# Optimization experiments

Measured on AMD Instinct MI355X. Metric: run time of the kernel, lower is better.

The kernel has to match this reference:

```python
import jax, jax.numpy as jnp
import numpy as np


def setup_inputs() -> dict:
    key = jax.random.key(0)
    k1, k2, k3, k4 = jax.random.split(key, 4)
    B, T, C, H = 16, 2048, 384, 64
    x = jax.random.normal(k1, (B, T, C), dtype=jnp.float32)
    Wq = jax.random.normal(k2, (C, H), dtype=jnp.float32) * (1.0 / np.sqrt(C))
    Wk = jax.random.normal(k3, (C, H), dtype=jnp.float32) * (1.0 / np.sqrt(C))
    Wv = jax.random.normal(k4, (C, H), dtype=jnp.float32) * (1.0 / np.sqrt(C))
    return {"x": x, "Wq": Wq, "Wk": Wk, "Wv": Wv}


def reference(x, Wq, Wk, Wv):
    # x: [B, T, C]; Wq/Wk/Wv: [C, H]
    T = x.shape[1]
    H = Wk.shape[1]
    q = jnp.einsum('btc,ch->bth', x, Wq)
    k = jnp.einsum('btc,ch->bth', x, Wk)
    v = jnp.einsum('btc,ch->bth', x, Wv)
    scale = 1.0 / jnp.sqrt(jnp.asarray(H, dtype=x.dtype))
    wei = jnp.einsum('bth,bsh->bts', q, k) * scale  # [B, T, T]
    causal = jnp.tril(jnp.ones((T, T), dtype=bool))
    wei = jnp.where(causal, wei, -jnp.inf)
    attn = jax.nn.softmax(wei, axis=-1)
    # dropout p=0 -> identity
    out = jnp.einsum('bts,bsh->bth', attn, v)  # [B, T, H]
    return out
```

## Files before the change

### kernel.cpp

```cpp
#include <hip/hip_runtime.h>
#include <hip/hip_bf16.h>

#define B_ 16
#define T_ 2048
#define C_ 384
#define H_ 64

typedef __attribute__((ext_vector_type(8))) short short8;
typedef __attribute__((ext_vector_type(4))) short short4_t;
typedef __attribute__((ext_vector_type(4))) float floatx4;
typedef __attribute__((ext_vector_type(2))) unsigned int uint2_t;
typedef __attribute__((ext_vector_type(4))) unsigned int uintx4;

#if defined(__has_builtin)
#if __has_builtin(__builtin_amdgcn_mfma_f32_16x16x16bf16_1k)
#define HAVE_MFMA16 1
#endif
#endif

static __device__ __forceinline__ short f2bf(float f) {
    unsigned u = __builtin_bit_cast(unsigned, f);
    u += 0x7FFF + ((u >> 16) & 1);
    return (short)(u >> 16);
}
static __device__ __forceinline__ float bf2f(short s) {
    return __builtin_bit_cast(float, ((unsigned)(unsigned short)s) << 16);
}
static __device__ __forceinline__ unsigned cvt_pk_bf16(float lo, float hi) {
    unsigned r;
    asm("v_cvt_pk_bf16_f32 %0, %1, %2" : "=v"(r) : "v"(lo), "v"(hi));
    return r;
}

__global__ void wt_kernel(const float* __restrict__ Wq, const float* __restrict__ Wk,
                          const float* __restrict__ Wv, short* __restrict__ wt2) {
    int idx = blockIdx.x * 256 + threadIdx.x;
    if (idx >= 12 * 12 * 512) return;
    int f = idx >> 9, within = idx & 511;
    int lane = within >> 3, jj = within & 7;
    int nt16 = f / 12, kc32 = f - nt16 * 12;
    int mat = nt16 >> 2, w = nt16 & 3;
    int quad = lane >> 4, l16 = lane & 15;
    int h = w * 16 + l16;
    int c = kc32 * 32 + quad * 8 + jj;
    const float* W = (mat == 0) ? Wq : ((mat == 1) ? Wk : Wv);
    wt2[idx] = f2bf(W[c * H_ + h]);
}

__global__ __launch_bounds__(256) void qkv_kernel(
        const float* __restrict__ x, const short* __restrict__ wt2,
        short* __restrict__ qo, short* __restrict__ ko, short* __restrict__ vto) {
    __shared__ short xs[64 * 392];

    int b = blockIdx.y, t0 = blockIdx.x * 64;
    int tid = threadIdx.x;

    const float* src = x + (size_t)(b * T_ + t0) * C_;
    for (int i = 0; i < 24; i++) {
        int chunk = i * 256 + tid;
        int row = chunk / 96, off = (chunk % 96) * 4;
        float4 f = *(const float4*)&src[row * 384 + off];
        uint2_t u2;
        u2.x = cvt_pk_bf16(f.x, f.y);
        u2.y = cvt_pk_bf16(f.z, f.w);
        *(uint2_t*)&xs[row * 392 + off] = u2;
    }
    __syncthreads();

    int w = tid >> 6, lane = tid & 63, quad = lane >> 4, l16 = lane & 15;

    floatx4 acc[4][3];
    for (int mt = 0; mt < 4; mt++)
        for (int j = 0; j < 3; j++) acc[mt][j] = (floatx4)0.0f;

    for (int kc = 0; kc < 384; kc += 32) {
        int kc32 = kc >> 5;
        short8 a[4];
        for (int mt = 0; mt < 4; mt++)
            a[mt] = *(const short8*)&xs[(mt * 16 + l16) * 392 + kc + quad * 8];
        for (int j = 0; j < 3; j++) {
            short8 bf = *(const short8*)&wt2[(((j * 4 + w) * 12) + kc32) * 512 + lane * 8];
            for (int mt = 0; mt < 4; mt++)
                acc[mt][j] = __builtin_amdgcn_mfma_f32_16x16x32_bf16(a[mt], bf, acc[mt][j], 0, 0, 0);
        }
    }
    __syncthreads();

    {
        int h = w * 16 + l16;
        for (int j = 0; j < 3; j++)
            for (int mt = 0; mt < 4; mt++)
                for (int r = 0; r < 4; r += 2) {
                    unsigned pk2 = cvt_pk_bf16(acc[mt][j][r], acc[mt][j][r + 1]);
                    int tl0 = mt * 16 + quad * 4 + r;
                    if (j == 0) {
                        xs[tl0 * 72 + h] = (short)pk2;
                        xs[(tl0 + 1) * 72 + h] = (short)(pk2 >> 16);
                    } else if (j == 1) {
                        xs[4608 + tl0 * 72 + h] = (short)pk2;
                        xs[4608 + (tl0 + 1) * 72 + h] = (short)(pk2 >> 16);
                    } else {
                        *(unsigned*)&xs[9216 + h * 72 + tl0] = pk2;
                    }
                }
    }
    __syncthreads();

    {
        int row = tid >> 3, off = (tid & 7) * 8;
        for (int i = 0; i < 2; i++) {
            int rr = row + i * 32;
            *(short8*)&qo[(size_t)(b * T_ + t0 + rr) * H_ + off] = *(const short8*)&xs[rr * 72 + off];
            *(short8*)&ko[(size_t)(b * T_ + t0 + rr) * H_ + off] = *(const short8*)&xs[4608 + rr * 72 + off];
        }
    }
    {
        int h = tid >> 2, off = (tid & 3) * 16;
        *(short8*)&vto[(size_t)(b * H_ + h) * T_ + t0 + off] = *(const short8*)&xs[9216 + h * 72 + off];
        *(short8*)&vto[(size_t)(b * H_ + h) * T_ + t0 + off + 8] = *(const short8*)&xs[9216 + h * 72 + off + 8];
    }
}

#define KVSZ (64 * 72)
#define SLOT_BYTES (16384 + 512)

__global__ __launch_bounds__(256) void attn_seg_kernel(
        const short* __restrict__ q, const short* __restrict__ k,
        const short* __restrict__ vt, float* __restrict__ slots) {
    __shared__ short ks[2 * KVSZ];
    __shared__ short vs[2 * KVSZ];
#if !defined(HAVE_MFMA16)
    __shared__ short ps[4 * 16 * 72];
#endif

    int b = blockIdx.y, fid = blockIdx.x, nslot = gridDim.x;
    int tt = 0, cum = 0;
    while (cum + ((2 * tt + 5) >> 2) <= fid) { cum += (2 * tt + 5) >> 2; tt++; }
    int nk = 2 * tt + 2;
    int k0 = (fid - cum) * 4;
    int k1 = min(k0 + 4, nk);

    int tid = threadIdx.x, w = tid >> 6, lane = tid & 63, quad = lane >> 4, l16 = lane & 15;
    int trow0 = tt * 128 + w * 32;

    short8 aq[2][2];
    for (int mt = 0; mt < 2; mt++) {
        const short* qrow = q + (size_t)(b * T_ + trow0 + mt * 16 + l16) * H_;
        aq[mt][0] = *(const short8*)&qrow[quad * 8];
        aq[mt][1] = *(const short8*)&qrow[32 + quad * 8];
    }

    floatx4 o[2][4];
    for (int mt = 0; mt < 2; mt++)
        for (int i = 0; i < 4; i++) o[mt][i] = (floatx4)0.0f;
    float lp[2] = {0.f, 0.f};

    const short* kb0 = k + (size_t)b * T_ * H_;
    const short* vtb = vt + (size_t)b * H_ * T_;

    int srow = tid >> 3, soff = (tid & 7) * 8;
    const float C1 = 0.125f * 1.44269504f;
    const float C2 = 12.0f * 1.44269504f;

    {
        const short* kg = kb0 + (size_t)k0 * 64 * H_;
        const short* vg = vtb + k0 * 64;
        *(short8*)&ks[srow * 72 + soff] = *(const short8*)&kg[srow * H_ + soff];
        *(short8*)&ks[(srow + 32) * 72 + soff] = *(const short8*)&kg[(srow + 32) * H_ + soff];
        *(short8*)&vs[srow * 72 + soff] = *(const short8*)&vg[(size_t)srow * T_ + soff];
        *(short8*)&vs[(srow + 32) * 72 + soff] = *(const short8*)&vg[(size_t)(srow + 32) * T_ + soff];
    }
    __syncthreads();

    int p = 0;
    for (int st = k0; st < k1; st++) {
        bool more = (st + 1 < k1);
        short8 pk0, pk1, pv0, pv1;
        if (more) {
            const short* kg = kb0 + (size_t)(st + 1) * 64 * H_;
            const short* vg = vtb + (st + 1) * 64;
            pk0 = *(const short8*)&kg[srow * H_ + soff];
            pk1 = *(const short8*)&kg[(srow + 32) * H_ + soff];
            pv0 = *(const short8*)&vg[(size_t)srow * T_ + soff];
            pv1 = *(const short8*)&vg[(size_t)(srow + 32) * T_ + soff];
        }
        const short* ksp = ks + p * KVSZ;
        const short* vsp = vs + p * KVSZ;
        int s0 = st * 64;

        floatx4 sacc[2][4];
        for (int mt = 0; mt < 2; mt++)
            for (int nt = 0; nt < 4; nt++) sacc[mt][nt] = (floatx4)0.0f;
        __builtin_amdgcn_s_setprio(1);
        for (int nt = 0; nt < 4; nt++) {
            short8 bk0 = *(const short8*)&ksp[(nt * 16 + l16) * 72 + quad * 8];
            short8 bk1 = *(const short8*)&ksp[(nt * 16 + l16) * 72 + 32 + quad * 8];
            sacc[0][nt] = __builtin_amdgcn_mfma_f32_16x16x32_bf16(bk0, aq[0][0], sacc[0][nt], 0, 0, 0);
            sacc[0][nt] = __builtin_amdgcn_mfma_f32_16x16x32_bf16(bk1, aq[0][1], sacc[0][nt], 0, 0, 0);
            sacc[1][nt] = __builtin_amdgcn_mfma_f32_16x16x32_bf16(bk0, aq[1][0], sacc[1][nt], 0, 0, 0);
            sacc[1][nt] = __builtin_amdgcn_mfma_f32_16x16x32_bf16(bk1, aq[1][1], sacc[1][nt], 0, 0, 0);
        }
        __builtin_amdgcn_s_setprio(0);

        bool diag = (st >= 2 * tt);
#if defined(HAVE_MFMA16)
        short4_t pa[2][4];
        if (!diag) {
            for (int mt = 0; mt < 2; mt++) {
                float ts[4];
                for (int nt = 0; nt < 4; nt++) {
                    float pv[4];
                    for (int r = 0; r < 4; r++)
                        pv[r] = __builtin_amdgcn_exp2f(fmaf(sacc[mt][nt][r], C1, -C2));
                    uint2_t u;
                    u.x = cvt_pk_bf16(pv[0], pv[1]);
                    u.y = cvt_pk_bf16(pv[2], pv[3]);
                    pa[mt][nt] = __builtin_bit_cast(short4_t, u);
                    ts[nt] = (pv[0] + pv[1]) + (pv[2] + pv[3]);
                }
                lp[mt] += (ts[0] + ts[1]) + (ts[2] + ts[3]);
            }
        } else {
            for (int mt = 0; mt < 2; mt++) {
                int q_idx = trow0 + mt * 16 + l16;
                float ts[4];
                for (int nt = 0; nt < 4; nt++) {
                    float pv[4];
                    for (int r = 0; r < 4; r++) {
                        float pe = __builtin_amdgcn_exp2f(fmaf(sacc[mt][nt][r], C1, -C2));
                        int s_idx = s0 + nt * 16 + quad * 4 + r;
                        pv[r] = (s_idx > q_idx) ? 0.0f : pe;
                    }
                    uint2_t u;
                    u.x = cvt_pk_bf16(pv[0], pv[1]);
                    u.y = cvt_pk_bf16(pv[2], pv[3]);
                    pa[mt][nt] = __builtin_bit_cast(short4_t, u);
                    ts[nt] = (pv[0] + pv[1]) + (pv[2] + pv[3]);
                }
                lp[mt] += (ts[0] + ts[1]) + (ts[2] + ts[3]);
            }
        }
        __builtin_amdgcn_s_setprio(1);
        for (int nh = 0; nh < 4; nh++) {
            const short* vrow = &vsp[(nh * 16 + l16) * 72 + quad * 4];
            for (int c = 0; c < 4; c++) {
                short4_t bv = *(const short4_t*)&vrow[c * 16];
                o[0][nh] = __builtin_amdgcn_mfma_f32_16x16x16bf16_1k(pa[0][c], bv, o[0][nh], 0, 0, 0);
                o[1][nh] = __builtin_amdgcn_mfma_f32_16x16x16bf16_1k(pa[1][c], bv, o[1][nh], 0, 0, 0);
            }
        }
        __builtin_amdgcn_s_setprio(0);
#else
        short* psw = ps + w * 16 * 72;
        short8 ap[2][2];
        for (int mt = 0; mt < 2; mt++) {
            int q_idx = trow0 + mt * 16 + l16;
            for (int nt = 0; nt < 4; nt++)
                for (int r = 0; r < 4; r++) {
                    float pv = __builtin_amdgcn_exp2f(fmaf(sacc[mt][nt][r], C1, -C2));
                    int s_idx = s0 + nt * 16 + quad * 4 + r;
                    if (diag && (s_idx > q_idx)) pv = 0.0f;
                    lp[mt] += pv;
                    psw[l16 * 72 + nt * 16 + quad * 4 + r] = f2bf(pv);
                }
            ap[mt][0] = *(const short8*)&psw[l16 * 72 + quad * 8];
            ap[mt][1] = *(const short8*)&psw[l16 * 72 + 32 + quad * 8];
        }
        for (int nh = 0; nh < 4; nh++) {
            short8 bv0 = *(const short8*)&vsp[(nh * 16 + l16) * 72 + quad * 8];
            short8 bv1 = *(const short8*)&vsp[(nh * 16 + l16) * 72 + 32 + quad * 8];
            o[0][nh] = __builtin_amdgcn_mfma_f32_16x16x32_bf16(ap[0][0], bv0, o[0][nh], 0, 0, 0);
            o[0][nh] = __builtin_amdgcn_mfma_f32_16x16x32_bf16(ap[0][1], bv1, o[0][nh], 0, 0, 0);
            o[1][nh] = __builtin_amdgcn_mfma_f32_16x16x32_bf16(ap[1][0], bv0, o[1][nh], 0, 0, 0);
            o[1][nh] = __builtin_amdgcn_mfma_f32_16x16x32_bf16(ap[1][1], bv1, o[1][nh], 0, 0, 0);
        }
#endif

        if (more) {
            short* kd = ks + (1 - p) * KVSZ;
            short* vd = vs + (1 - p) * KVSZ;
            *(short8*)&kd[srow * 72 + soff] = pk0;
            *(short8*)&kd[(srow + 32) * 72 + soff] = pk1;
            *(short8*)&vd[srow * 72 + soff] = pv0;
            *(short8*)&vd[(srow + 32) * 72 + soff] = pv1;
            __syncthreads();
            p ^= 1;
        }
    }

    for (int mt = 0; mt < 2; mt++) {
        lp[mt] += __shfl_xor(lp[mt], 16);
        lp[mt] += __shfl_xor(lp[mt], 32);
    }

    char* slotb = (char*)slots + ((size_t)b * nslot + fid) * SLOT_BYTES;
    short* slotO = (short*)slotb;
    float* slotL = (float*)(slotb + 16384);

    for (int mt = 0; mt < 2; mt++)
        for (int nh = 0; nh < 4; nh++)
            for (int r = 0; r < 4; r += 2) {
                unsigned pk2 = cvt_pk_bf16(o[mt][nh][r], o[mt][nh][r + 1]);
                slotO[(w * 32 + mt * 16 + quad * 4 + r) * 64 + nh * 16 + l16] = (short)pk2;
                slotO[(w * 32 + mt * 16 + quad * 4 + r + 1) * 64 + nh * 16 + l16] = (short)(pk2 >> 16);
            }
    if (quad == 0)
        for (int mt = 0; mt < 2; mt++)
            slotL[w * 32 + mt * 16 + l16] = lp[mt];
}

__global__ __launch_bounds__(256) void combine_kernel(
        const float* __restrict__ slots, int nslot, float* __restrict__ out) {
    int b = blockIdx.y, tb = blockIdx.x;
    int tt = tb >> 1;
    int nseg = (2 * tt + 5) >> 2;
    int cum = 0;
    for (int i = 0; i < tt; i++) cum += (2 * i + 5) >> 2;
    const char* base = (const char*)slots + ((size_t)b * nslot + cum) * SLOT_BYTES;

    int tid = threadIdx.x;
    int row = (tb & 1) * 64 + (tid >> 2);
    int qo = (tid & 3) * 16;
    float acc[16];
    for (int i = 0; i < 16; i++) acc[i] = 0.f;
    float lsum = 0.f;
    for (int s = 0; s < nseg; s++) {
        const short* O = (const short*)(base + (size_t)s * SLOT_BYTES);
        const float* L = (const float*)(base + (size_t)s * SLOT_BYTES + 16384);
        for (int i = 0; i < 2; i++) {
            short8 v = *(const short8*)&O[row * 64 + qo + i * 8];
            uintx4 u = __builtin_bit_cast(uintx4, v);
            for (int j = 0; j < 4; j++) {
                acc[i * 8 + 2 * j]     += __builtin_bit_cast(float, u[j] << 16);
                acc[i * 8 + 2 * j + 1] += __builtin_bit_cast(float, u[j] & 0xFFFF0000u);
            }
        }
        lsum += L[row];
    }
    float inv = 1.0f / lsum;
    float* op = out + (size_t)(b * T_ + tt * 128 + row) * H_ + qo;
    for (int i = 0; i < 4; i++) {
        float4 v;
        v.x = acc[i * 4 + 0] * inv; v.y = acc[i * 4 + 1] * inv;
        v.z = acc[i * 4 + 2] * inv; v.w = acc[i * 4 + 3] * inv;
        *(float4*)&op[i * 4] = v;
    }
}

template<bool DIAG>
static __device__ __forceinline__ void attn_step(
        int s0, int t0w, int quad, int l16,
        const short* __restrict__ kbase, const short* __restrict__ vtb,
        short8 aq0, short8 aq1, short* __restrict__ psw,
        floatx4 (&o)[4], float (&lpart)[4]) {
    floatx4 sacc[4];
    for (int nt = 0; nt < 4; nt++) sacc[nt] = (floatx4)0.0f;
    for (int nt = 0; nt < 4; nt++) {
        short8 bk0 = *(const short8*)&kbase[(nt * 16 + l16) * H_ + quad * 8];
        short8 bk1 = *(const short8*)&kbase[(nt * 16 + l16) * H_ + 32 + quad * 8];
        sacc[nt] = __builtin_amdgcn_mfma_f32_16x16x32_bf16(aq0, bk0, sacc[nt], 0, 0, 0);
        sacc[nt] = __builtin_amdgcn_mfma_f32_16x16x32_bf16(aq1, bk1, sacc[nt], 0, 0, 0);
    }
    const float C1 = 0.125f * 1.44269504f;
    const float C2 = 12.0f * 1.44269504f;
    for (int nt = 0; nt < 4; nt++) {
        int s_idx = s0 + nt * 16 + l16;
        for (int r = 0; r < 4; r++) {
            float p = __builtin_amdgcn_exp2f(fmaf(sacc[nt][r], C1, -C2));
            if (DIAG && (s_idx > t0w + quad * 4 + r)) p = 0.0f;
            lpart[r] += p;
            psw[(quad * 4 + r) * 72 + nt * 16 + l16] = f2bf(p);
        }
    }
    short8 ap0 = *(const short8*)&psw[l16 * 72 + quad * 8];
    short8 ap1 = *(const short8*)&psw[l16 * 72 + 32 + quad * 8];
    for (int nh = 0; nh < 4; nh++) {
        short8 bv0 = *(const short8*)&vtb[(size_t)(nh * 16 + l16) * T_ + s0 + quad * 8];
        short8 bv1 = *(const short8*)&vtb[(size_t)(nh * 16 + l16) * T_ + s0 + 32 + quad * 8];
        o[nh] = __builtin_amdgcn_mfma_f32_16x16x32_bf16(ap0, bv0, o[nh], 0, 0, 0);
        o[nh] = __builtin_amdgcn_mfma_f32_16x16x32_bf16(ap1, bv1, o[nh], 0, 0, 0);
    }
}

__global__ __launch_bounds__(256) void attn_kernel(
        const short* __restrict__ q, const short* __restrict__ k,
        const short* __restrict__ vt, float* __restrict__ out) {
    __shared__ short ps[4 * 16 * 72];

    int b = blockIdx.y;
    int g = ((int)blockIdx.x + 4 * (b & 7)) & 31;
    int tt = (b < 8) ? g : 31 - g;
    int t0 = tt * 64;
    int tid = threadIdx.x, w = tid >> 6, lane = tid & 63, quad = lane >> 4, l16 = lane & 15;
    int t0w = t0 + w * 16;

    const short* qrow = q + (size_t)(b * T_ + t0w + l16) * H_;
    short8 aq0 = *(const short8*)&qrow[quad * 8];
    short8 aq1 = *(const short8*)&qrow[32 + quad * 8];

    floatx4 o[4];
    for (int nh = 0; nh < 4; nh++) o[nh] = (floatx4)0.0f;
    float lpart[4] = {0.f, 0.f, 0.f, 0.f};

    const short* kb0 = k + (size_t)b * T_ * H_;
    const short* vtb = vt + (size_t)b * H_ * T_;
    short* psw = ps + w * 16 * 72;

    for (int st = 0; st < tt; st++)
        attn_step<false>(st * 64, t0w, quad, l16, kb0 + (size_t)st * 64 * H_,
                         vtb, aq0, aq1, psw, o, lpart);
    attn_step<true>(tt * 64, t0w, quad, l16, kb0 + (size_t)tt * 64 * H_,
                    vtb, aq0, aq1, psw, o, lpart);

    for (int d = 1; d < 16; d <<= 1)
        for (int r = 0; r < 4; r++)
            lpart[r] += __shfl_xor(lpart[r], d, 16);

    for (int nh = 0; nh < 4; nh++)
        for (int r = 0; r < 4; r++) {
            int t = t0w + quad * 4 + r;
            out[(size_t)(b * T_ + t) * H_ + nh * 16 + l16] = o[nh][r] / lpart[r];
        }
}

extern "C" void kernel_launch(void* const* d_in, const int* in_sizes, int n_in,
                              void* d_out, int out_size, void* d_ws, size_t ws_size,
                              hipStream_t stream) {
    const float* x  = (const float*)d_in[0];
    const float* Wq = (const float*)d_in[1];
    const float* Wk = (const float*)d_in[2];
    const float* Wv = (const float*)d_in[3];

    char* ws = (char*)d_ws;
    short* qb  = (short*)(ws);
    short* kb  = (short*)(ws + (size_t)4 * 1024 * 1024);
    short* vtb = (short*)(ws + (size_t)8 * 1024 * 1024);
    short* wtb = (short*)(ws + (size_t)12 * 1024 * 1024);
    float* slots = (float*)(ws + (size_t)12 * 1024 * 1024 + 256 * 1024);
    size_t base_need = (size_t)12 * 1024 * 1024 + 256 * 1024;

    wt_kernel<<<dim3(288), dim3(256), 0, stream>>>(Wq, Wk, Wv, wtb);
    qkv_kernel<<<dim3(T_ / 64, B_), dim3(256), 0, stream>>>(x, wtb, qb, kb, vtb);

    float* out = (float*)d_out;
    const int NSLOT = 72;
    if (ws_size >= base_need + (size_t)B_ * NSLOT * (size_t)SLOT_BYTES) {
        attn_seg_kernel<<<dim3(NSLOT, B_), dim3(256), 0, stream>>>(qb, kb, vtb, slots);
        combine_kernel<<<dim3(T_ / 64, B_), dim3(256), 0, stream>>>(slots, NSLOT, out);
    } else {
        attn_kernel<<<dim3(T_ / 64, B_), dim3(256), 0, stream>>>(qb, kb, vtb, out);
    }
}
```

Baseline: 129.9 us.

## Single-buffer KV LDS, raise occupancy, reverse segment order, finer combine grid

The attention segment kernel drops its double-buffered K/V shared memory to a single buffer and adds a second barrier before overwriting it. Launch bounds now request 6 waves per SIMD, so more blocks can be resident at once. Block indices are reversed so the heavier diagonal-row segments are scheduled first. The combine kernel is split into twice as many blocks, each handling 32 rows with 8 columns per thread. The cost is an extra barrier per step and losing overlap between LDS stores and compute, and the tighter register cap may cause spills.

```diff
diff --git a/kernel.cpp b/kernel.cpp
--- a/kernel.cpp
+++ b/kernel.cpp
@@ -124,16 +124,17 @@
 #define KVSZ (64 * 72)
 #define SLOT_BYTES (16384 + 512)
 
-__global__ __launch_bounds__(256) void attn_seg_kernel(
+__global__ __launch_bounds__(256, 6) void attn_seg_kernel(
         const short* __restrict__ q, const short* __restrict__ k,
         const short* __restrict__ vt, float* __restrict__ slots) {
-    __shared__ short ks[2 * KVSZ];
-    __shared__ short vs[2 * KVSZ];
+    __shared__ short ks[KVSZ];
+    __shared__ short vs[KVSZ];
 #if !defined(HAVE_MFMA16)
     __shared__ short ps[4 * 16 * 72];
 #endif
 
-    int b = blockIdx.y, fid = blockIdx.x, nslot = gridDim.x;
+    int nslot = gridDim.x;
+    int b = blockIdx.y, fid = nslot - 1 - (int)blockIdx.x;
     int tt = 0, cum = 0;
     while (cum + ((2 * tt + 5) >> 2) <= fid) { cum += (2 * tt + 5) >> 2; tt++; }
     int nk = 2 * tt + 2;
@@ -172,7 +173,6 @@
     }
     __syncthreads();
 
-    int p = 0;
     for (int st = k0; st < k1; st++) {
         bool more = (st + 1 < k1);
         short8 pk0, pk1, pv0, pv1;
@@ -184,8 +184,6 @@
             pv0 = *(const short8*)&vg[(size_t)srow * T_ + soff];
             pv1 = *(const short8*)&vg[(size_t)(srow + 32) * T_ + soff];
         }
-        const short* ksp = ks + p * KVSZ;
-        const short* vsp = vs + p * KVSZ;
         int s0 = st * 64;
 
         floatx4 sacc[2][4];
@@ -193,8 +191,8 @@
             for (int nt = 0; nt < 4; nt++) sacc[mt][nt] = (floatx4)0.0f;
         __builtin_amdgcn_s_setprio(1);
         for (int nt = 0; nt < 4; nt++) {
-            short8 bk0 = *(const short8*)&ksp[(nt * 16 + l16) * 72 + quad * 8];
-            short8 bk1 = *(const short8*)&ksp[(nt * 16 + l16) * 72 + 32 + quad * 8];
+            short8 bk0 = *(const short8*)&ks[(nt * 16 + l16) * 72 + quad * 8];
+            short8 bk1 = *(const short8*)&ks[(nt * 16 + l16) * 72 + 32 + quad * 8];
             sacc[0][nt] = __builtin_amdgcn_mfma_f32_16x16x32_bf16(bk0, aq[0][0], sacc[0][nt], 0, 0, 0);
             sacc[0][nt] = __builtin_amdgcn_mfma_f32_16x16x32_bf16(bk1, aq[0][1], sacc[0][nt], 0, 0, 0);
             sacc[1][nt] = __builtin_amdgcn_mfma_f32_16x16x32_bf16(bk0, aq[1][0], sacc[1][nt], 0, 0, 0);
@@ -242,7 +240,7 @@
         }
         __builtin_amdgcn_s_setprio(1);
         for (int nh = 0; nh < 4; nh++) {
-            const short* vrow = &vsp[(nh * 16 + l16) * 72 + quad * 4];
+            const short* vrow = &vs[(nh * 16 + l16) * 72 + quad * 4];
             for (int c = 0; c < 4; c++) {
                 short4_t bv = *(const short4_t*)&vrow[c * 16];
                 o[0][nh] = __builtin_amdgcn_mfma_f32_16x16x16bf16_1k(pa[0][c], bv, o[0][nh], 0, 0, 0);
@@ -267,8 +265,8 @@
             ap[mt][1] = *(const short8*)&psw[l16 * 72 + 32 + quad * 8];
         }
         for (int nh = 0; nh < 4; nh++) {
-            short8 bv0 = *(const short8*)&vsp[(nh * 16 + l16) * 72 + quad * 8];
-            short8 bv1 = *(const short8*)&vsp[(nh * 16 + l16) * 72 + 32 + quad * 8];
+            short8 bv0 = *(const short8*)&vs[(nh * 16 + l16) * 72 + quad * 8];
+            short8 bv1 = *(const short8*)&vs[(nh * 16 + l16) * 72 + 32 + quad * 8];
             o[0][nh] = __builtin_amdgcn_mfma_f32_16x16x32_bf16(ap[0][0], bv0, o[0][nh], 0, 0, 0);
             o[0][nh] = __builtin_amdgcn_mfma_f32_16x16x32_bf16(ap[0][1], bv1, o[0][nh], 0, 0, 0);
             o[1][nh] = __builtin_amdgcn_mfma_f32_16x16x32_bf16(ap[1][0], bv0, o[1][nh], 0, 0, 0);
@@ -277,14 +275,12 @@
 #endif
 
         if (more) {
-            short* kd = ks + (1 - p) * KVSZ;
-            short* vd = vs + (1 - p) * KVSZ;
-            *(short8*)&kd[srow * 72 + soff] = pk0;
-            *(short8*)&kd[(srow + 32) * 72 + soff] = pk1;
-            *(short8*)&vd[srow * 72 + soff] = pv0;
-            *(short8*)&vd[(srow + 32) * 72 + soff] = pv1;
             __syncthreads();
-            p ^= 1;
+            *(short8*)&ks[srow * 72 + soff] = pk0;
+            *(short8*)&ks[(srow + 32) * 72 + soff] = pk1;
+            *(short8*)&vs[srow * 72 + soff] = pv0;
+            *(short8*)&vs[(srow + 32) * 72 + soff] = pv1;
+            __syncthreads();
         }
     }
 
@@ -312,34 +308,32 @@
 __global__ __launch_bounds__(256) void combine_kernel(
         const float* __restrict__ slots, int nslot, float* __restrict__ out) {
     int b = blockIdx.y, tb = blockIdx.x;
-    int tt = tb >> 1;
+    int tt = tb >> 2;
     int nseg = (2 * tt + 5) >> 2;
     int cum = 0;
     for (int i = 0; i < tt; i++) cum += (2 * i + 5) >> 2;
     const char* base = (const char*)slots + ((size_t)b * nslot + cum) * SLOT_BYTES;
 
     int tid = threadIdx.x;
-    int row = (tb & 1) * 64 + (tid >> 2);
-    int qo = (tid & 3) * 16;
-    float acc[16];
-    for (int i = 0; i < 16; i++) acc[i] = 0.f;
+    int row = (tb & 3) * 32 + (tid >> 3);
+    int qo = (tid & 7) * 8;
+    float acc[8];
+    for (int i = 0; i < 8; i++) acc[i] = 0.f;
     float lsum = 0.f;
     for (int s = 0; s < nseg; s++) {
         const short* O = (const short*)(base + (size_t)s * SLOT_BYTES);
         const float* L = (const float*)(base + (size_t)s * SLOT_BYTES + 16384);
-        for (int i = 0; i < 2; i++) {
-            short8 v = *(const short8*)&O[row * 64 + qo + i * 8];
-            uintx4 u = __builtin_bit_cast(uintx4, v);
-            for (int j = 0; j < 4; j++) {
-                acc[i * 8 + 2 * j]     += __builtin_bit_cast(float, u[j] << 16);
-                acc[i * 8 + 2 * j + 1] += __builtin_bit_cast(float, u[j] & 0xFFFF0000u);
-            }
+        short8 v = *(const short8*)&O[row * 64 + qo];
+        uintx4 u = __builtin_bit_cast(uintx4, v);
+        for (int j = 0; j < 4; j++) {
+            acc[2 * j]     += __builtin_bit_cast(float, u[j] << 16);
+            acc[2 * j + 1] += __builtin_bit_cast(float, u[j] & 0xFFFF0000u);
         }
         lsum += L[row];
     }
     float inv = 1.0f / lsum;
     float* op = out + (size_t)(b * T_ + tt * 128 + row) * H_ + qo;
-    for (int i = 0; i < 4; i++) {
+    for (int i = 0; i < 2; i++) {
         float4 v;
         v.x = acc[i * 4 + 0] * inv; v.y = acc[i * 4 + 1] * inv;
         v.z = acc[i * 4 + 2] * inv; v.w = acc[i * 4 + 3] * inv;
@@ -446,7 +440,7 @@
     const int NSLOT = 72;
     if (ws_size >= base_need + (size_t)B_ * NSLOT * (size_t)SLOT_BYTES) {
         attn_seg_kernel<<<dim3(NSLOT, B_), dim3(256), 0, stream>>>(qb, kb, vtb, slots);
-        combine_kernel<<<dim3(T_ / 64, B_), dim3(256), 0, stream>>>(slots, NSLOT, out);
+        combine_kernel<<<dim3(T_ / 32, B_), dim3(256), 0, stream>>>(slots, NSLOT, out);
     } else {
         attn_kernel<<<dim3(T_ / 64, B_), dim3(256), 0, stream>>>(qb, kb, vtb, out);
     }
```

Result: slower. 187.9 us (+44.7%).
